# Kernel optimization log

Hardware: AMD Instinct MI355X
Metric: run time of the kernel (lower is better)

## Reference

```python
import jax, jax.numpy as jnp
import numpy as np

B, L = 128, 200
NUM_C, D, M = 10000, 128, 64


def setup_inputs() -> dict:
    key = jax.random.key(0)
    ks = jax.random.split(key, 16)
    n = lambda k, s, sc=0.05: jax.random.normal(k, s, dtype=jnp.float32) * sc
    return {
        "q": jax.random.randint(ks[0], (B, L), 0, NUM_C),
        "r": jax.random.randint(ks[1], (B, L), 0, 2),
        "k_emb": n(ks[2], (NUM_C, D)),
        "v_emb": n(ks[3], (2, D)),
        "Mk": n(ks[4], (M, D), 0.2),   # kaiming_normal_
        "Mv0": n(ks[5], (M, D), 0.2),  # kaiming_normal_
        "f_W": n(ks[6], (D, 2 * D)), "f_b": jnp.zeros((D,), jnp.float32),
        "e_W": n(ks[7], (D, D)), "e_b": jnp.zeros((D,), jnp.float32),
        "a_W": n(ks[8], (D, D)), "a_b": jnp.zeros((D,), jnp.float32),
        "ab_W": n(ks[9], (1, D)), "ab_b": jnp.zeros((1,), jnp.float32),
        "df_W": n(ks[10], (1, D)), "df_b": jnp.zeros((1,), jnp.float32),
    }


def reference(q, r, k_emb, v_emb, Mk, Mv0, f_W, f_b, e_W, e_b, a_W, a_b, ab_W, ab_b, df_W, df_b):
    # Embeddings
    k = k_emb[q]                # [B, L, D] question key embedding
    v = k + v_emb[r]            # [B, L, D] value embedding

    # Attention over memory slots, erase/add gates
    w = jax.nn.softmax(jnp.einsum('bld,md->blm', k, Mk), axis=-1)   # [B, L, M]
    e = jax.nn.sigmoid(jnp.einsum('bld,ed->ble', v, e_W) + e_b)      # erase [B, L, D]
    a = jnp.tanh(jnp.einsum('bld,ed->ble', v, a_W) + a_b)            # add   [B, L, D]

    Mvt0 = jnp.broadcast_to(Mv0[None], (q.shape[0], Mv0.shape[0], Mv0.shape[1]))  # [B, M, D]

    def step(Mvt, inp):
        wt, et, at = inp  # [B,M], [B,D], [B,D]
        # read uses memory BEFORE this timestep's write (Mv[:, :-1] in torch)
        read = jnp.einsum('bm,bmd->bd', wt, Mvt)
        we = wt[:, :, None]
        Mvt_new = Mvt * (1.0 - we * et[:, None, :]) + we * at[:, None, :]
        return Mvt_new, read

    _, reads = jax.lax.scan(
        step, Mvt0,
        (w.transpose(1, 0, 2), e.transpose(1, 0, 2), a.transpose(1, 0, 2)))
    reads = reads.transpose(1, 0, 2)  # [B, L, D]

    f = jnp.tanh(jnp.concatenate([reads, k], axis=-1) @ f_W.T + f_b)  # [B, L, D]
    stu_ability = jnp.tanh(f @ ab_W.T + ab_b)   # [B, L, 1] (dropout is identity in eval)
    que_diff = jnp.tanh(k @ df_W.T + df_b)      # [B, L, 1]
    p = jax.nn.sigmoid(3.0 * stu_ability - que_diff)
    return p.squeeze(-1)  # [B, L]
```

## Files before the change

kernel.cpp:

```cpp
#include <hip/hip_runtime.h>

typedef unsigned short ushort_t;
typedef _Float16 f16_t;
typedef _Float16 f16x2 __attribute__((ext_vector_type(2)));
typedef short bf16x8 __attribute__((ext_vector_type(8)));
typedef float f32x4 __attribute__((ext_vector_type(4)));

#define B_ 128
#define L_ 200
#define D_ 128
#define M_ 64

__device__ __forceinline__ float fast_sigmoid(float x) {
    return 1.f / (1.f + __expf(-x));
}

__device__ __forceinline__ float fast_tanh(float x) {
    float xc = fminf(fmaxf(x, -15.f), 15.f);
    float e = __expf(2.f * xc);
    return (e - 1.f) / (e + 1.f);
}

__device__ __forceinline__ ushort_t f2bf(float f) {
    union { float f; unsigned int u; } x;
    x.f = f;
    unsigned int u = x.u;
    unsigned int r = (u + 0x7FFFu + ((u >> 16) & 1u)) >> 16;
    return (ushort_t)r;
}

__device__ __forceinline__ uint4 pack8(float4 a, float4 b) {
    uint4 u;
    u.x = (unsigned)f2bf(a.x) | ((unsigned)f2bf(a.y) << 16);
    u.y = (unsigned)f2bf(a.z) | ((unsigned)f2bf(a.w) << 16);
    u.z = (unsigned)f2bf(b.x) | ((unsigned)f2bf(b.y) << 16);
    u.w = (unsigned)f2bf(b.z) | ((unsigned)f2bf(b.w) << 16);
    return u;
}

__device__ __forceinline__ unsigned pack_ea(float e, float a) {
    union { f16_t h[2]; unsigned u; } p;
    p.h[0] = (f16_t)e;
    p.h[1] = (f16_t)a;
    return p.u;
}

__device__ __forceinline__ f16x2 u2h2(unsigned u) {
    union { unsigned u; f16x2 h; } x;
    x.u = u;
    return x.h;
}

#if __has_builtin(__builtin_amdgcn_fdot2)
#define FDOT2(a, b, c) __builtin_amdgcn_fdot2((a), (b), (c), false)
#else
#define FDOT2(a, b, c) ((c) + (float)(a).x * (float)(b).x + (float)(a).y * (float)(b).y)
#endif

#define F_WQ   0u
#define F_EAQ  1638400u
#define F_FKQ  8192000u
#define F_RD   11468800u
#define F_DIFF 14745600u
#define F_PACK 14771200u
#define WPACK_N 59392
#define FPACK_N 16384

__global__ __launch_bounds__(256) void k_pack(
    const float* __restrict__ Mk, const float* __restrict__ eW,
    const float* __restrict__ aW, const float* __restrict__ fW,
    const float* __restrict__ dfW,
    ushort_t* __restrict__ Wpack, ushort_t* __restrict__ Fpack)
{
    int i = blockIdx.x * 256 + threadIdx.x;
    if (i < WPACK_N) {
        int g = i >> 9, lane = (i >> 3) & 63, j = i & 7;
        int nt = g >> 2, ks = g & 3;
        int col = nt * 16 + (lane & 15);
        int d = ks * 32 + ((lane >> 4) << 3) + j;
        float v;
        if (col < 64)       v = Mk[col * 128 + d];
        else if (col < 192) v = eW[(col - 64) * 128 + d];
        else if (col < 320) v = aW[(col - 192) * 128 + d];
        else if (col < 448) v = fW[(col - 320) * 256 + 128 + d];
        else                v = (col == 448) ? dfW[d] : 0.f;
        Wpack[i] = f2bf(v);
    } else if (i < WPACK_N + FPACK_N) {
        int e = i - WPACK_N;
        int g = e >> 9, lane = (e >> 3) & 63, j = e & 7;
        int nt = g >> 2, ks = g & 3;
        int col = nt * 16 + (lane & 15);
        int d = ks * 32 + ((lane >> 4) << 3) + j;
        Fpack[e] = f2bf(fW[col * 256 + d]);
    }
}

__device__ __forceinline__ void loadB4(const ushort_t* __restrict__ base,
                                       int nt, int lane, bf16x8* b) {
    const ushort_t* p = base + (nt * 256 + lane) * 8;
    b[0] = *(const bf16x8*)(p);
    b[1] = *(const bf16x8*)(p + 512);
    b[2] = *(const bf16x8*)(p + 1024);
    b[3] = *(const bf16x8*)(p + 1536);
}

__global__ __launch_bounds__(512) void k_pre_mfma(
    const int* __restrict__ q, const int* __restrict__ r,
    const float* __restrict__ k_emb, const float* __restrict__ v_emb,
    const ushort_t* __restrict__ Wpack,
    const float* __restrict__ e_b, const float* __restrict__ a_b,
    const float* __restrict__ df_b,
    f16_t* __restrict__ wq, unsigned* __restrict__ eaq,
    f16_t* __restrict__ fkq, float* __restrict__ diffq)
{
    __shared__ ushort_t skA[8192];
    __shared__ ushort_t svA[8192];
    __shared__ float slog[64 * 68];

    const int tid = threadIdx.x;
    const int pos0 = blockIdx.x * 64;
    const int wave = tid >> 6;
    const int lane = tid & 63;
    const int mt = wave & 3;
    const int nh = wave >> 2;

    #pragma unroll
    for (int i = 0; i < 2; i++) {
        int E = tid + 512 * i;
        int mtile = E >> 8, ks = (E >> 6) & 3, le = E & 63;
        int prow = pos0 + mtile * 16 + (le & 15);
        int dof = ks * 32 + ((le >> 4) << 3);
        int qv = q[prow], rv = r[prow];
        const float4* kp = (const float4*)(k_emb + qv * 128 + dof);
        float4 ka = kp[0], kb = kp[1];
        const float4* vp = (const float4*)(v_emb + rv * 128 + dof);
        float4 va = vp[0], vb = vp[1];
        *(uint4*)&skA[E * 8] = pack8(ka, kb);
        float4 s0, s1;
        s0.x = ka.x + va.x; s0.y = ka.y + va.y; s0.z = ka.z + va.z; s0.w = ka.w + va.w;
        s1.x = kb.x + vb.x; s1.y = kb.y + vb.y; s1.z = kb.z + vb.z; s1.w = kb.w + vb.w;
        *(uint4*)&svA[E * 8] = pack8(s0, s1);
    }
    __syncthreads();

    bf16x8 A[4];
    {
        const ushort_t* src = nh ? svA : skA;
        #pragma unroll
        for (int ks = 0; ks < 4; ks++)
            A[ks] = *(const bf16x8*)&src[((mt * 4 + ks) * 64 + lane) * 8];
    }

    const int col = lane & 15;
    const int quad = lane >> 4;
    const int rbase = mt * 16 + quad * 4;

    if (nh == 0) {
        bf16x8 Bb[2][4];
        loadB4(Wpack, 0, lane, Bb[0]);
        #pragma unroll
        for (int j = 0; j < 13; j++) {
            if (j < 12) {
                int jn = j + 1;
                loadB4(Wpack, (jn < 4) ? jn : jn + 16, lane, Bb[jn & 1]);
            }
            f32x4 acc = {0.f, 0.f, 0.f, 0.f};
            #pragma unroll
            for (int ks = 0; ks < 4; ks++)
                acc = __builtin_amdgcn_mfma_f32_16x16x32_bf16(A[ks], Bb[j & 1][ks], acc, 0, 0, 0);
            if (j < 4) {
                #pragma unroll
                for (int reg = 0; reg < 4; reg++)
                    slog[(rbase + reg) * 68 + j * 16 + col] = acc[reg];
            } else if (j < 12) {
                int base = (((blockIdx.x * 4 + mt) * 8 + (j - 4)) * 4) * 64;
                #pragma unroll
                for (int reg = 0; reg < 4; reg++)
                    fkq[base + reg * 64 + lane] = (f16_t)acc[reg];
            } else {
                if (col == 0) {
                    float db = df_b[0];
                    #pragma unroll
                    for (int reg = 0; reg < 4; reg++)
                        diffq[pos0 + rbase + reg] = fast_tanh(acc[reg] + db);
                }
            }
        }
        {
            int row = tid >> 2, ln = tid & 3;
            const float* lr = slog + row * 68 + ln * 16;
            float v[16];
            #pragma unroll
            for (int j = 0; j < 16; j++) v[j] = lr[j];
            float mx = v[0];
            #pragma unroll
            for (int j = 1; j < 16; j++) mx = fmaxf(mx, v[j]);
            mx = fmaxf(mx, __shfl_xor(mx, 1));
            mx = fmaxf(mx, __shfl_xor(mx, 2));
            float s = 0.f;
            #pragma unroll
            for (int j = 0; j < 16; j++) { v[j] = __expf(v[j] - mx); s += v[j]; }
            s += __shfl_xor(s, 1); s += __shfl_xor(s, 2);
            float inv = 1.f / s;
            union { f16_t h[8]; uint4 u; } o0, o1;
            #pragma unroll
            for (int j = 0; j < 8; j++) o0.h[j] = (f16_t)(v[j] * inv);
            #pragma unroll
            for (int j = 0; j < 8; j++) o1.h[j] = (f16_t)(v[8 + j] * inv);
            f16_t* wout = wq + (pos0 + row) * 64 + ln * 16;
            *(uint4*)(wout) = o0.u;
            *(uint4*)(wout + 8) = o1.u;
        }
    } else {
        bf16x8 Be[2][4], Ba[2][4];
        loadB4(Wpack, 4, lane, Be[0]);
        loadB4(Wpack, 12, lane, Ba[0]);
        #pragma unroll
        for (int i = 0; i < 8; i++) {
            if (i < 7) {
                loadB4(Wpack, 5 + i, lane, Be[(i + 1) & 1]);
                loadB4(Wpack, 13 + i, lane, Ba[(i + 1) & 1]);
            }
            f32x4 ae = {0.f, 0.f, 0.f, 0.f};
            f32x4 aa = {0.f, 0.f, 0.f, 0.f};
            #pragma unroll
            for (int ks = 0; ks < 4; ks++) {
                ae = __builtin_amdgcn_mfma_f32_16x16x32_bf16(A[ks], Be[i & 1][ks], ae, 0, 0, 0);
                aa = __builtin_amdgcn_mfma_f32_16x16x32_bf16(A[ks], Ba[i & 1][ks], aa, 0, 0, 0);
            }
            int c = i * 16 + col;
            float ebv = e_b[c], abv = a_b[c];
            #pragma unroll
            for (int reg = 0; reg < 4; reg++) {
                float ev = fast_sigmoid(ae[reg] + ebv);
                float av = fast_tanh(aa[reg] + abv);
                eaq[(pos0 + rbase + reg) * 128 + c] = pack_ea(ev, av);
            }
        }
    }
}

#define SC_PREFETCH(wX, eX, cN)                                            \
    _Pragma("unroll")                                                      \
    for (int tt = 0; tt < 8; tt++) {                                       \
        wX[tt] = wh4[((cN) * 8 + tt) * 8 + sc];                            \
        eX[tt] = eab[((cN) * 8 + tt) * 128];                               \
    }

#define SC_COMPUTE(wX, eX, bb)                                             \
    _Pragma("unroll")                                                      \
    for (int tt = 0; tt < 8; tt++) {                                       \
        uint4 wp = wX[tt];                                                 \
        f16x2 w01 = u2h2(wp.x), w23 = u2h2(wp.y);                          \
        f16x2 w45 = u2h2(wp.z), w67 = u2h2(wp.w);                          \
        f16x2 ea = u2h2(eX[tt]);                                           \
        f16x2 ee = __builtin_shufflevector(ea, ea, 0, 0);                  \
        f16x2 av = __builtin_shufflevector(ea, ea, 1, 1);                  \
        float r0 = FDOT2(w01, Mv[0], 0.f);                                 \
        float r1 = FDOT2(w45, Mv[2], 0.f);                                 \
        r0 = FDOT2(w23, Mv[1], r0);                                        \
        r1 = FDOT2(w67, Mv[3], r1);                                        \
        Mv[0] = __builtin_elementwise_fma(w01,                             \
                    __builtin_elementwise_fma(-ee, Mv[0], av), Mv[0]);     \
        Mv[1] = __builtin_elementwise_fma(w23,                             \
                    __builtin_elementwise_fma(-ee, Mv[1], av), Mv[1]);     \
        Mv[2] = __builtin_elementwise_fma(w45,                             \
                    __builtin_elementwise_fma(-ee, Mv[2], av), Mv[2]);     \
        Mv[3] = __builtin_elementwise_fma(w67,                             \
                    __builtin_elementwise_fma(-ee, Mv[3], av), Mv[3]);     \
        pbuf[bb][sc][tt][lane] = r0 + r1;                                  \
    }

#define SC_REDUCE(bb, c0) {                                                \
        float s = pbuf[bb][0][wv][lane] + pbuf[bb][1][wv][lane]            \
                + pbuf[bb][2][wv][lane] + pbuf[bb][3][wv][lane]            \
                + pbuf[bb][4][wv][lane] + pbuf[bb][5][wv][lane]            \
                + pbuf[bb][6][wv][lane] + pbuf[bb][7][wv][lane];           \
        rbase[((c0) * 8 + wv) * 128 + lane] = f2bf(s);                     \
    }

__global__ __launch_bounds__(512, 2) void k_scan(
    const f16_t* __restrict__ wq, const unsigned* __restrict__ eaq,
    const float* __restrict__ Mv0, ushort_t* __restrict__ reads)
{
    __shared__ float pbuf[2][8][8][64];

    const int tid = threadIdx.x;
    const int b = blockIdx.x >> 1;
    const int dh = blockIdx.x & 1;
    const int wv = tid >> 6;
    const int sc = __builtin_amdgcn_readfirstlane(wv);
    const int lane = tid & 63;
    const int d = dh * 64 + lane;

    f16x2 Mv[4];
    #pragma unroll
    for (int j = 0; j < 4; j++) {
        f16x2 m;
        m.x = (f16_t)Mv0[(sc * 8 + 2 * j) * D_ + d];
        m.y = (f16_t)Mv0[(sc * 8 + 2 * j + 1) * D_ + d];
        Mv[j] = m;
    }

    const uint4* wh4 = (const uint4*)(wq + b * (L_ * M_));
    const unsigned* eab = eaq + b * (L_ * 128) + d;
    ushort_t* rbase = reads + b * (L_ * D_) + dh * 64;

    uint4 wA[8], wB[8];
    unsigned eA[8], eB[8];

    SC_PREFETCH(wA, eA, 0);

    for (int cc = 0; cc < 12; cc++) {
        const int c0 = 2 * cc;
        SC_PREFETCH(wB, eB, c0 + 1);
        SC_COMPUTE(wA, eA, 0);
        __syncthreads();
        SC_REDUCE(0, c0);
        SC_PREFETCH(wA, eA, c0 + 2);
        SC_COMPUTE(wB, eB, 1);
        __syncthreads();
        SC_REDUCE(1, c0 + 1);
    }
    SC_COMPUTE(wA, eA, 0);
    __syncthreads();
    SC_REDUCE(0, 24);
}

__global__ __launch_bounds__(512) void k_final_mfma(
    const ushort_t* __restrict__ reads, const f16_t* __restrict__ fkq,
    const float* __restrict__ diffq, const ushort_t* __restrict__ Fpack,
    const float* __restrict__ f_b, const float* __restrict__ ab_W,
    const float* __restrict__ ab_b, float* __restrict__ out)
{
    __shared__ float sab[64 * 2];

    const int tid = threadIdx.x;
    const int pos0 = blockIdx.x * 64;
    const int wave = tid >> 6;
    const int lane = tid & 63;
    const int mt = wave & 3;
    const int half = wave >> 2;

    const int col = lane & 15;
    const int quad = lane >> 4;
    const int rbase = mt * 16 + quad * 4;

    bf16x8 A[4];
    {
        const ushort_t* arow = reads
            + (pos0 + mt * 16 + (lane & 15)) * 128 + ((lane >> 4) << 3);
        #pragma unroll
        for (int ks = 0; ks < 4; ks++)
            A[ks] = *(const bf16x8*)(arow + ks * 32);
    }

    float fkv[16];
    #pragma unroll
    for (int i = 0; i < 4; i++) {
        int base = (((blockIdx.x * 4 + mt) * 8 + (half * 4 + i)) * 4) * 64;
        #pragma unroll
        for (int reg = 0; reg < 4; reg++)
            fkv[i * 4 + reg] = (float)fkq[base + reg * 64 + lane];
    }

    float abacc[4] = {0.f, 0.f, 0.f, 0.f};

    bf16x8 Bb[2][4];
    loadB4(Fpack, half * 4, lane, Bb[0]);
    #pragma unroll
    for (int i = 0; i < 4; i++) {
        if (i < 3) loadB4(Fpack, half * 4 + i + 1, lane, Bb[(i + 1) & 1]);
        f32x4 acc = {0.f, 0.f, 0.f, 0.f};
        #pragma unroll
        for (int ks = 0; ks < 4; ks++)
            acc = __builtin_amdgcn_mfma_f32_16x16x32_bf16(A[ks], Bb[i & 1][ks], acc, 0, 0, 0);
        int c = (half * 4 + i) * 16 + col;
        float fb = f_b[c];
        float abw = ab_W[c];
        #pragma unroll
        for (int reg = 0; reg < 4; reg++) {
            float fv = fast_tanh(acc[reg] + fkv[i * 4 + reg] + fb);
            abacc[reg] = fmaf(abw, fv, abacc[reg]);
        }
    }

    #pragma unroll
    for (int reg = 0; reg < 4; reg++) {
        float v = abacc[reg];
        v += __shfl_xor(v, 1); v += __shfl_xor(v, 2);
        v += __shfl_xor(v, 4); v += __shfl_xor(v, 8);
        abacc[reg] = v;
    }
    if (col == 0) {
        #pragma unroll
        for (int reg = 0; reg < 4; reg++)
            sab[(rbase + reg) * 2 + half] = abacc[reg];
    }
    __syncthreads();
    if (tid < 64) {
        float ab = fast_tanh(sab[tid * 2] + sab[tid * 2 + 1] + ab_b[0]);
        int pos = pos0 + tid;
        out[pos] = fast_sigmoid(3.f * ab - diffq[pos]);
    }
}

extern "C" void kernel_launch(void* const* d_in, const int* in_sizes, int n_in,
                              void* d_out, int out_size, void* d_ws, size_t ws_size,
                              hipStream_t stream)
{
    const int*   q     = (const int*)d_in[0];
    const int*   r     = (const int*)d_in[1];
    const float* k_emb = (const float*)d_in[2];
    const float* v_emb = (const float*)d_in[3];
    const float* Mk    = (const float*)d_in[4];
    const float* Mv0   = (const float*)d_in[5];
    const float* f_W   = (const float*)d_in[6];
    const float* f_b   = (const float*)d_in[7];
    const float* e_W   = (const float*)d_in[8];
    const float* e_b   = (const float*)d_in[9];
    const float* a_W   = (const float*)d_in[10];
    const float* a_b   = (const float*)d_in[11];
    const float* ab_W  = (const float*)d_in[12];
    const float* ab_b  = (const float*)d_in[13];
    const float* df_W  = (const float*)d_in[14];
    const float* df_b  = (const float*)d_in[15];

    float* ws = (float*)d_ws;
    float* out = (float*)d_out;
    f16_t*    wq_h    = (f16_t*)(ws + F_WQ);
    unsigned* eaq_u   = (unsigned*)(ws + F_EAQ);
    f16_t*    fkq_h   = (f16_t*)(ws + F_FKQ);
    ushort_t* reads_b = (ushort_t*)(ws + F_RD);
    ushort_t* Wpack = (ushort_t*)(ws + F_PACK);
    ushort_t* Fpack = Wpack + WPACK_N;

    k_pack<<<296, 256, 0, stream>>>(Mk, e_W, a_W, f_W, df_W, Wpack, Fpack);

    k_pre_mfma<<<400, 512, 0, stream>>>(
        q, r, k_emb, v_emb, Wpack, e_b, a_b, df_b,
        wq_h, eaq_u, fkq_h, ws + F_DIFF);

    k_scan<<<256, 512, 0, stream>>>(
        wq_h, eaq_u, Mv0, reads_b);

    k_final_mfma<<<400, 512, 0, stream>>>(
        reads_b, fkq_h, ws + F_DIFF, Fpack,
        f_b, ab_W, ab_b, out);
}
```

Baseline: 137.6 us.

## Stage packed weight tiles through shared memory in precompute kernel

The projection precompute kernel now cooperatively loads each packed weight tile from global memory into a double-buffered shared-memory region once per block. Previously each wave fetched its own B fragments straight from global memory. Both halves of the block (the key-logit/f-key path and the erase/add path) run a unified 16-step loop with a block barrier per step. This cuts redundant global weight traffic across the waves, at the cost of 16 block-wide syncs and lockstep execution of two paths that do unequal amounts of work.

```diff
diff --git a/kernel.cpp b/kernel.cpp
--- a/kernel.cpp
+++ b/kernel.cpp
@@ -150,93 +150,119 @@
         for (int ks = 0; ks < 4; ks++)
             A[ks] = *(const bf16x8*)&src[((mt * 4 + ks) * 64 + lane) * 8];
     }
+    __syncthreads();
+
+    ushort_t* sB = skA;
+
+    {
+        int slot = tid >> 8, t = tid & 255;
+        int nt = slot ? 4 : 0;
+        *(uint4*)&sB[slot * 2048 + t * 8] = *(const uint4*)&Wpack[nt * 2048 + t * 8];
+    }
+    __syncthreads();
 
     const int col = lane & 15;
     const int quad = lane >> 4;
     const int rbase = mt * 16 + quad * 4;
 
-    if (nh == 0) {
-        bf16x8 Bb[2][4];
-        loadB4(Wpack, 0, lane, Bb[0]);
-        #pragma unroll
-        for (int j = 0; j < 13; j++) {
-            if (j < 12) {
-                int jn = j + 1;
-                loadB4(Wpack, (jn < 4) ? jn : jn + 16, lane, Bb[jn & 1]);
+    f32x4 ae = {0.f, 0.f, 0.f, 0.f};
+
+    #pragma unroll
+    for (int j = 0; j < 16; j++) {
+        if (j < 15) {
+            int jn = j + 1;
+            int slot = tid >> 8, t = tid & 255;
+            int nt = slot ? ((jn & 1) ? 12 + (jn >> 1) : 4 + (jn >> 1))
+                          : (jn < 4 ? jn : (jn < 12 ? jn + 16 : 28));
+            *(uint4*)&sB[((jn & 1) * 2 + slot) * 2048 + t * 8] =
+                *(const uint4*)&Wpack[nt * 2048 + t * 8];
+        }
+        if (nh == 0) {
+            if (j < 13) {
+                bf16x8 Bb[4];
+                {
+                    const ushort_t* p = &sB[((j & 1) * 2 + 0) * 2048 + lane * 8];
+                    Bb[0] = *(const bf16x8*)(p);
+                    Bb[1] = *(const bf16x8*)(p + 512);
+                    Bb[2] = *(const bf16x8*)(p + 1024);
+                    Bb[3] = *(const bf16x8*)(p + 1536);
+                }
+                f32x4 acc = {0.f, 0.f, 0.f, 0.f};
+                #pragma unroll
+                for (int ks = 0; ks < 4; ks++)
+                    acc = __builtin_amdgcn_mfma_f32_16x16x32_bf16(A[ks], Bb[ks], acc, 0, 0, 0);
+                if (j < 4) {
+                    #pragma unroll
+                    for (int reg = 0; reg < 4; reg++)
+                        slog[(rbase + reg) * 68 + j * 16 + col] = acc[reg];
+                } else if (j < 12) {
+                    int base = (((blockIdx.x * 4 + mt) * 8 + (j - 4)) * 4) * 64;
+                    #pragma unroll
+                    for (int reg = 0; reg < 4; reg++)
+                        fkq[base + reg * 64 + lane] = (f16_t)acc[reg];
+                } else {
+                    if (col == 0) {
+                        float db = df_b[0];
+                        #pragma unroll
+                        for (int reg = 0; reg < 4; reg++)
+                            diffq[pos0 + rbase + reg] = fast_tanh(acc[reg] + db);
+                    }
+                }
+            }
+        } else {
+            bf16x8 Bb[4];
+            {
+                const ushort_t* p = &sB[((j & 1) * 2 + 1) * 2048 + lane * 8];
+                Bb[0] = *(const bf16x8*)(p);
+                Bb[1] = *(const bf16x8*)(p + 512);
+                Bb[2] = *(const bf16x8*)(p + 1024);
+                Bb[3] = *(const bf16x8*)(p + 1536);
             }
             f32x4 acc = {0.f, 0.f, 0.f, 0.f};
             #pragma unroll
             for (int ks = 0; ks < 4; ks++)
-                acc = __builtin_amdgcn_mfma_f32_16x16x32_bf16(A[ks], Bb[j & 1][ks], acc, 0, 0, 0);
-            if (j < 4) {
+                acc = __builtin_amdgcn_mfma_f32_16x16x32_bf16(A[ks], Bb[ks], acc, 0, 0, 0);
+            if ((j & 1) == 0) {
+                ae = acc;
+            } else {
+                int i = j >> 1;
+                int c = i * 16 + col;
+                float ebv = e_b[c], abv = a_b[c];
                 #pragma unroll
-                for (int reg = 0; reg < 4; reg++)
-                    slog[(rbase + reg) * 68 + j * 16 + col] = acc[reg];
-            } else if (j < 12) {
-                int base = (((blockIdx.x * 4 + mt) * 8 + (j - 4)) * 4) * 64;
-                #pragma unroll
-                for (int reg = 0; reg < 4; reg++)
-                    fkq[base + reg * 64 + lane] = (f16_t)acc[reg];
-            } else {
-                if (col == 0) {
-                    float db = df_b[0];
-                    #pragma unroll
-                    for (int reg = 0; reg < 4; reg++)
-                        diffq[pos0 + rbase + reg] = fast_tanh(acc[reg] + db);
+                for (int reg = 0; reg < 4; reg++) {
+                    float ev = fast_sigmoid(ae[reg] + ebv);
+                    float av = fast_tanh(acc[reg] + abv);
+                    eaq[(pos0 + rbase + reg) * 128 + c] = pack_ea(ev, av);
                 }
             }
         }
-        {
-            int row = tid >> 2, ln = tid & 3;
-            const float* lr = slog + row * 68 + ln * 16;
-            float v[16];
-            #pragma unroll
-            for (int j = 0; j < 16; j++) v[j] = lr[j];
-            float mx = v[0];
-            #pragma unroll
-            for (int j = 1; j < 16; j++) mx = fmaxf(mx, v[j]);
-            mx = fmaxf(mx, __shfl_xor(mx, 1));
-            mx = fmaxf(mx, __shfl_xor(mx, 2));
-            float s = 0.f;
-            #pragma unroll
-            for (int j = 0; j < 16; j++) { v[j] = __expf(v[j] - mx); s += v[j]; }
-            s += __shfl_xor(s, 1); s += __shfl_xor(s, 2);
-            float inv = 1.f / s;
-            union { f16_t h[8]; uint4 u; } o0, o1;
-            #pragma unroll
-            for (int j = 0; j < 8; j++) o0.h[j] = (f16_t)(v[j] * inv);
-            #pragma unroll
-            for (int j = 0; j < 8; j++) o1.h[j] = (f16_t)(v[8 + j] * inv);
-            f16_t* wout = wq + (pos0 + row) * 64 + ln * 16;
-            *(uint4*)(wout) = o0.u;
-            *(uint4*)(wout + 8) = o1.u;
-        }
-    } else {
-        bf16x8 Be[2][4], Ba[2][4];
-        loadB4(Wpack, 4, lane, Be[0]);
-        loadB4(Wpack, 12, lane, Ba[0]);
-        #pragma unroll
-        for (int i = 0; i < 8; i++) {
-            if (i < 7) {
-                loadB4(Wpack, 5 + i, lane, Be[(i + 1) & 1]);
-                loadB4(Wpack, 13 + i, lane, Ba[(i + 1) & 1]);
-            }
-            f32x4 ae = {0.f, 0.f, 0.f, 0.f};
-            f32x4 aa = {0.f, 0.f, 0.f, 0.f};
-            #pragma unroll
-            for (int ks = 0; ks < 4; ks++) {
-                ae = __builtin_amdgcn_mfma_f32_16x16x32_bf16(A[ks], Be[i & 1][ks], ae, 0, 0, 0);
-                aa = __builtin_amdgcn_mfma_f32_16x16x32_bf16(A[ks], Ba[i & 1][ks], aa, 0, 0, 0);
-            }
-            int c = i * 16 + col;
-            float ebv = e_b[c], abv = a_b[c];
-            #pragma unroll
-            for (int reg = 0; reg < 4; reg++) {
-                float ev = fast_sigmoid(ae[reg] + ebv);
-                float av = fast_tanh(aa[reg] + abv);
-                eaq[(pos0 + rbase + reg) * 128 + c] = pack_ea(ev, av);
-            }
-        }
+        __syncthreads();
+    }
+
+    if (nh == 0) {
+        int row = tid >> 2, ln = tid & 3;
+        const float* lr = slog + row * 68 + ln * 16;
+        float v[16];
+        #pragma unroll
+        for (int j = 0; j < 16; j++) v[j] = lr[j];
+        float mx = v[0];
+        #pragma unroll
+        for (int j = 1; j < 16; j++) mx = fmaxf(mx, v[j]);
+        mx = fmaxf(mx, __shfl_xor(mx, 1));
+        mx = fmaxf(mx, __shfl_xor(mx, 2));
+        float s = 0.f;
+        #pragma unroll
+        for (int j = 0; j < 16; j++) { v[j] = __expf(v[j] - mx); s += v[j]; }
+        s += __shfl_xor(s, 1); s += __shfl_xor(s, 2);
+        float inv = 1.f / s;
+        union { f16_t h[8]; uint4 u; } o0, o1;
+        #pragma unroll
+        for (int j = 0; j < 8; j++) o0.h[j] = (f16_t)(v[j] * inv);
+        #pragma unroll
+        for (int j = 0; j < 8; j++) o1.h[j] = (f16_t)(v[8 + j] * inv);
+        f16_t* wout = wq + (pos0 + row) * 64 + ln * 16;
+        *(uint4*)(wout) = o0.u;
+        *(uint4*)(wout + 8) = o1.u;
     }
 }
 
```

After: 141.6 us. 2.9% more time.
